# Kernel optimization log

Hardware: AMD Instinct MI355X
Metric: run time of the kernel (lower is better)

The kernel has to match this reference:

```python
import jax, jax.numpy as jnp
import numpy as np

N = 50000
E = 800000
IN_DIM = 256
OUT_DIM = 64
ALPHA = 0.2  # LeakyReLU negative slope
EPS = 9e-15


def setup_inputs() -> dict:
    key = jax.random.key(0)
    k1, k2, k3, k4 = jax.random.split(key, 4)
    x = jax.random.normal(k1, (N, IN_DIM), dtype=jnp.float32)
    edge = jax.random.randint(k2, (2, E), 0, N, dtype=jnp.int32)
    # xavier_normal with gain=1.414
    gain = 1.414
    W = jax.random.normal(k3, (IN_DIM, OUT_DIM), dtype=jnp.float32) * (gain * np.sqrt(2.0 / (IN_DIM + OUT_DIM)))
    attn = jax.random.normal(k4, (1, 2 * OUT_DIM), dtype=jnp.float32) * (gain * np.sqrt(2.0 / (1 + 2 * OUT_DIM)))
    return {"x": x, "edge": edge, "W": W, "attn": attn}


def reference(x, edge, W, attn):
    n = x.shape[0]
    h = x @ W                                   # [N, D]
    src, dst = edge[0], edge[1]
    d = h.shape[1]
    a_src = attn[0, :d]                         # attn . concat(h_src, h_dst) split
    a_dst = attn[0, d:]
    s = h @ a_src                               # [N]
    t = h @ a_dst                               # [N]
    values = s[src] + t[dst]                    # [E] per-edge attention logits
    edge_e_a = jnp.where(values >= 0, values, ALPHA * values)  # LeakyReLU
    edge_e = jnp.exp(edge_e_a - jnp.max(edge_e_a))              # [E]
    # scatter-sum over destination rows (edge[0] is the output row in spmm)
    e_rowsum = jax.ops.segment_sum(edge_e, src, num_segments=n)[:, None]  # [N,1]
    msgs = edge_e[:, None] * h[dst]             # [E, D] gathered messages
    h_prime = jax.ops.segment_sum(msgs, src, num_segments=n)              # [N, D]
    h_prime = h_prime / (e_rowsum + EPS)
    return h_prime
```

## Files before the change

kernel.cpp:

```cpp
#include <hip/hip_runtime.h>
#include <stdint.h>

#define NN 50000
#define NE 800000
#define KDIM 256
#define DDIM 64
#define ALPHA 0.2f
#define EPSV 9e-15f

#define NBIN 512
#define BSPAN 98
#define SPAN2 49
#define BCAP 2048
#define HCAP 1024
#define PBLK 256
#define EPB 3125
#define GEMM_BLOCKS 512
#define FGRID (PBLK + GEMM_BLOCKS)

#define O_S    0
#define O_T    50000
#define O_HB   100000
#define O_WB   1700000
#define O_BIN  1708192
#define O_EBUF 1708704

typedef __bf16 bf16x8 __attribute__((ext_vector_type(8)));
typedef float f32x4 __attribute__((ext_vector_type(4)));

__device__ __forceinline__ ushort f2bf(float f) {
    uint32_t u = __float_as_uint(f);
    return (ushort)((u + 0x7fffu + ((u >> 16) & 1u)) >> 16);
}
__device__ __forceinline__ float bf2f(ushort u) {
    return __uint_as_float(((uint32_t)u) << 16);
}
__device__ __forceinline__ uint binof(uint src) {
    return (src * 85599u) >> 23;
}

__global__ __launch_bounds__(256) void k_prep(const float* __restrict__ W,
                                              uint* __restrict__ BINCNT,
                                              uint4* __restrict__ WB) {
    const int g = blockIdx.x * 256 + threadIdx.x;
    if (g < NBIN) BINCNT[g] = 0u;
    if (g < 2048) {
        int ts = g >> 6;
        int ln = g & 63;
        int s = ts >> 2, t = ts & 3;
        int q = ln >> 4, c = ln & 15;
        union { ushort us[8]; uint4 v; } pk;
#pragma unroll
        for (int j = 0; j < 8; ++j) {
            int k = s * 32 + q * 8 + j;
            pk.us[j] = f2bf(W[k * DDIM + t * 16 + c]);
        }
        WB[g] = pk.v;
    }
}

__global__ __launch_bounds__(512) void k_fused(const float* __restrict__ X,
                                               const uint4* __restrict__ WB,
                                               const float* __restrict__ attn,
                                               const int* __restrict__ edge,
                                               ushort* __restrict__ HB,
                                               float* __restrict__ S,
                                               float* __restrict__ T,
                                               uint* __restrict__ BINCNT,
                                               uint* __restrict__ EBUF) {
    __shared__ uint4 bsm[2048];

    if (blockIdx.x < PBLK) {
        uint* sm = (uint*)bsm;
        const int CNT0 = 0, BST = 512, GBS = 1024, STG = 1536, SRT = 4672;
        const int tid = threadIdx.x;
        const int p0 = blockIdx.x * EPB;
        for (int b = tid; b < NBIN; b += 512) sm[CNT0 + b] = 0u;
        __syncthreads();
        for (int k = tid; k < EPB; k += 512) {
            uint s = (uint)edge[p0 + k];
            uint d = (uint)edge[NE + p0 + k];
            sm[STG + k] = s | (d << 16);
            atomicAdd(&sm[CNT0 + binof(s)], 1u);
        }
        __syncthreads();
        if (tid < 64) {
            uint carry = 0;
            for (int c = 0; c < 8; ++c) {
                uint v = sm[CNT0 + c * 64 + tid];
                uint incl = v;
#pragma unroll
                for (int m = 1; m < 64; m <<= 1) {
                    uint t = __shfl_up(incl, m, 64);
                    if (tid >= m) incl += t;
                }
                sm[BST + c * 64 + tid] = incl - v + carry;
                carry += __shfl(incl, 63, 64);
            }
        }
        __syncthreads();
        for (int b = tid; b < NBIN; b += 512) {
            uint c = sm[CNT0 + b];
            sm[GBS + b] = c ? atomicAdd(&BINCNT[b], c) : 0u;
            sm[CNT0 + b] = sm[BST + b];
        }
        __syncthreads();
        for (int k = tid; k < EPB; k += 512) {
            uint pk = sm[STG + k];
            uint bin = binof(pk & 0xffffu);
            uint slot = atomicAdd(&sm[CNT0 + bin], 1u);
            sm[SRT + slot] = pk;
        }
        __syncthreads();
        for (int k = tid; k < EPB; k += 512) {
            uint pk = sm[SRT + k];
            uint bin = binof(pk & 0xffffu);
            uint local = (uint)k - sm[BST + bin] + sm[GBS + bin];
            if (local < BCAP) EBUF[bin * BCAP + local] = pk;
        }
        return;
    }

    uint4 wreg[4];
#pragma unroll
    for (int j = 0; j < 4; ++j) wreg[j] = WB[j * 512 + threadIdx.x];
#pragma unroll
    for (int j = 0; j < 4; ++j) bsm[j * 512 + threadIdx.x] = wreg[j];
    __syncthreads();

    const int lane = threadIdx.x & 63;
    const int wave = (blockIdx.x - PBLK) * 8 + (threadIdx.x >> 6);
    const int nwaves = GEMM_BLOCKS * 8;
    const int quad = lane >> 4;
    const int nn = lane & 15;

    float asrc[4], adst[4];
#pragma unroll
    for (int t = 0; t < 4; ++t) {
        asrc[t] = attn[t * 16 + nn];
        adst[t] = attn[DDIM + t * 16 + nn];
    }

    const int MT = NN / 16;
    for (int mt = wave; mt < MT; mt += nwaves) {
        const int row0 = mt * 16;
        const float* xr = X + (size_t)(row0 + nn) * KDIM + quad * 8;
        bf16x8 afrag[8];
#pragma unroll
        for (int s = 0; s < 8; ++s) {
            float4 lo = *reinterpret_cast<const float4*>(xr + s * 32);
            float4 hi = *reinterpret_cast<const float4*>(xr + s * 32 + 4);
            union { uint u[4]; bf16x8 v; } aa;
            asm("v_cvt_pk_bf16_f32 %0, %1, %2"
                : "=v"(aa.u[0]) : "v"(lo.x), "v"(lo.y));
            asm("v_cvt_pk_bf16_f32 %0, %1, %2"
                : "=v"(aa.u[1]) : "v"(lo.z), "v"(lo.w));
            asm("v_cvt_pk_bf16_f32 %0, %1, %2"
                : "=v"(aa.u[2]) : "v"(hi.x), "v"(hi.y));
            asm("v_cvt_pk_bf16_f32 %0, %1, %2"
                : "=v"(aa.u[3]) : "v"(hi.z), "v"(hi.w));
            afrag[s] = aa.v;
        }

        f32x4 acc[4];
#pragma unroll
        for (int t = 0; t < 4; ++t) acc[t] = {0.f, 0.f, 0.f, 0.f};
#pragma unroll
        for (int s = 0; s < 8; ++s)
#pragma unroll
            for (int t = 0; t < 4; ++t) {
                bf16x8 bf = *reinterpret_cast<const bf16x8*>(
                    &bsm[(s * 4 + t) * 64 + lane]);
                acc[t] = __builtin_amdgcn_mfma_f32_16x16x32_bf16(
                    afrag[s], bf, acc[t], 0, 0, 0);
            }

#pragma unroll
        for (int t = 0; t < 4; ++t)
#pragma unroll
            for (int r = 0; r < 4; ++r)
                HB[(size_t)(row0 + quad * 4 + r) * DDIM + t * 16 + nn] =
                    f2bf(acc[t][r]);

        float sp[4], tp[4];
#pragma unroll
        for (int r = 0; r < 4; ++r) { sp[r] = 0.f; tp[r] = 0.f; }
#pragma unroll
        for (int t = 0; t < 4; ++t)
#pragma unroll
            for (int r = 0; r < 4; ++r) {
                sp[r] = fmaf(acc[t][r], asrc[t], sp[r]);
                tp[r] = fmaf(acc[t][r], adst[t], tp[r]);
            }
#pragma unroll
        for (int m = 1; m < 16; m <<= 1)
#pragma unroll
            for (int r = 0; r < 4; ++r) {
                sp[r] += __shfl_xor(sp[r], m, 64);
                tp[r] += __shfl_xor(tp[r], m, 64);
            }
        if (nn == 0) {
#pragma unroll
            for (int r = 0; r < 4; ++r) {
                S[row0 + quad * 4 + r] = sp[r];
                T[row0 + quad * 4 + r] = tp[r];
            }
        }
    }
}

__global__ __launch_bounds__(512) void k_agg(const uint* __restrict__ EBUF,
                                             const uint* __restrict__ BINCNT,
                                             const float* __restrict__ S,
                                             const float* __restrict__ T,
                                             const ushort* __restrict__ HB,
                                             float* __restrict__ out) {
    __shared__ uint2 sDE[HCAP];
    __shared__ uint  cntL[SPAN2];
    __shared__ uint  off[SPAN2 + 1];
    __shared__ uint  cur[SPAN2];
    __shared__ float Sseg[SPAN2];

    const int b = blockIdx.x >> 1;
    const int half = blockIdx.x & 1;
    const int nb0 = b * BSPAN + half * SPAN2;
    const int tid = threadIdx.x;

    if (tid < SPAN2) {
        cntL[tid] = 0u;
        int node = nb0 + tid;
        Sseg[tid] = (node < NN) ? S[node] : 0.f;
    }
    __syncthreads();

    int cnt = (int)BINCNT[b];
    cnt = cnt < BCAP ? cnt : BCAP;
    const uint* eb = EBUF + b * BCAP;

    for (int k = tid; k < cnt; k += 512) {
        int row = (int)(eb[k] & 0xffffu) - nb0;
        if ((unsigned)row < SPAN2) atomicAdd(&cntL[row], 1u);
    }
    __syncthreads();

    if (tid < 64) {
        uint v = (tid < SPAN2) ? cntL[tid] : 0u;
        uint incl = v;
#pragma unroll
        for (int m = 1; m < 64; m <<= 1) {
            uint t = __shfl_up(incl, m, 64);
            if (tid >= m) incl += t;
        }
        if (tid < SPAN2) { off[tid] = incl - v; cur[tid] = incl - v; }
        if (tid == SPAN2 - 1) off[SPAN2] = incl;
    }
    __syncthreads();

    for (int k = tid; k < cnt; k += 512) {
        uint pk = eb[k];
        int row = (int)(pk & 0xffffu) - nb0;
        if ((unsigned)row < SPAN2) {
            float v = Sseg[row] + T[pk >> 16];
            float a = v >= 0.f ? v : ALPHA * v;
            float e = __expf(a);
            uint pos = atomicAdd(&cur[row], 1u);
            sDE[pos] = make_uint2(pk >> 16, __float_as_uint(e));
        }
    }
    __syncthreads();

    const int wv = tid >> 6;
    const int lane = tid & 63;
    const int sub4 = lane >> 4;
    const int c4 = lane & 15;
    const ushort* hb4 = HB + 4 * c4;

    for (int r = wv; r < SPAN2; r += 8) {
        const int start = (int)off[r];
        const int deg = (int)(off[r + 1] - off[r]);
        float a0 = 0.f, a1 = 0.f, a2 = 0.f, a3 = 0.f, rs = 0.f;
        for (int j = 0; j < deg; j += 16) {
            uint dd[4]; float ee[4];
#pragma unroll
            for (int u = 0; u < 4; ++u) {
                int idx = j + 4 * u + sub4;
                int ic = start + (idx < deg ? idx : 0);
                uint2 q = sDE[ic];
                dd[u] = q.x;
                ee[u] = (idx < deg) ? __uint_as_float(q.y) : 0.f;
            }
            __builtin_amdgcn_sched_barrier(0);
            uint2 g[4];
#pragma unroll
            for (int u = 0; u < 4; ++u)
                g[u] = *reinterpret_cast<const uint2*>(
                    hb4 + (size_t)dd[u] * DDIM);
            __builtin_amdgcn_sched_barrier(0);
#pragma unroll
            for (int u = 0; u < 4; ++u) {
                a0 = fmaf(ee[u], bf2f((ushort)(g[u].x & 0xffffu)), a0);
                a1 = fmaf(ee[u], bf2f((ushort)(g[u].x >> 16)), a1);
                a2 = fmaf(ee[u], bf2f((ushort)(g[u].y & 0xffffu)), a2);
                a3 = fmaf(ee[u], bf2f((ushort)(g[u].y >> 16)), a3);
                rs += ee[u];
            }
        }
#pragma unroll
        for (int m = 16; m < 64; m <<= 1) {
            a0 += __shfl_xor(a0, m, 64);
            a1 += __shfl_xor(a1, m, 64);
            a2 += __shfl_xor(a2, m, 64);
            a3 += __shfl_xor(a3, m, 64);
            rs += __shfl_xor(rs, m, 64);
        }
        const int node = nb0 + r;
        if (sub4 == 0 && node < NN) {
            float inv = 1.f / (rs + EPSV);
            float4 o = make_float4(a0 * inv, a1 * inv, a2 * inv, a3 * inv);
            *reinterpret_cast<float4*>(out + (size_t)node * DDIM + 4 * c4) = o;
        }
    }
}

extern "C" void kernel_launch(void* const* d_in, const int* in_sizes, int n_in,
                              void* d_out, int out_size, void* d_ws, size_t ws_size,
                              hipStream_t stream) {
    const float* X    = (const float*)d_in[0];
    const int*   edge = (const int*)d_in[1];
    const float* W    = (const float*)d_in[2];
    const float* attn = (const float*)d_in[3];

    uint*   wu = (uint*)d_ws;
    float*  wf = (float*)d_ws;
    float*  S      = wf + O_S;
    float*  T      = wf + O_T;
    ushort* HB     = (ushort*)(wu + O_HB);
    uint4*  WB     = (uint4*)(wu + O_WB);
    uint*   BINCNT = wu + O_BIN;
    uint*   EBUF   = wu + O_EBUF;

    k_prep<<<8, 256, 0, stream>>>(W, BINCNT, WB);
    k_fused<<<FGRID, 512, 0, stream>>>(X, WB, attn, edge, HB, S, T, BINCNT, EBUF);
    k_agg<<<NBIN * 2, 512, 0, stream>>>(EBUF, BINCNT, S, T, HB, (float*)d_out);
}
```

Baseline: 122.8 us.

## Drop local sort in edge binning and double gather unroll in aggregation

The partition blocks no longer compute a prefix scan and local counting sort before writing edges to global bins. Each edge now takes its global slot directly from a shared atomic cursor seeded with the global bin offset, which removes one scan, two barriers and a shared-memory pass. Writes to EBUF become less contiguous and in-bin order becomes nondeterministic. Separately, the aggregation loop issues eight gathers per iteration instead of four, raising memory-level parallelism at the cost of more registers.

Result: slower. 126.4 us (+2.9%).

```diff
diff --git a/kernel.cpp b/kernel.cpp
--- a/kernel.cpp
+++ b/kernel.cpp
@@ -72,7 +72,7 @@
 
     if (blockIdx.x < PBLK) {
         uint* sm = (uint*)bsm;
-        const int CNT0 = 0, BST = 512, GBS = 1024, STG = 1536, SRT = 4672;
+        const int CNT0 = 0, CUR = 512, STG = 1024;
         const int tid = threadIdx.x;
         const int p0 = blockIdx.x * EPB;
         for (int b = tid; b < NBIN; b += 512) sm[CNT0 + b] = 0u;
@@ -84,39 +84,16 @@
             atomicAdd(&sm[CNT0 + binof(s)], 1u);
         }
         __syncthreads();
-        if (tid < 64) {
-            uint carry = 0;
-            for (int c = 0; c < 8; ++c) {
-                uint v = sm[CNT0 + c * 64 + tid];
-                uint incl = v;
-#pragma unroll
-                for (int m = 1; m < 64; m <<= 1) {
-                    uint t = __shfl_up(incl, m, 64);
-                    if (tid >= m) incl += t;
-                }
-                sm[BST + c * 64 + tid] = incl - v + carry;
-                carry += __shfl(incl, 63, 64);
-            }
-        }
-        __syncthreads();
         for (int b = tid; b < NBIN; b += 512) {
             uint c = sm[CNT0 + b];
-            sm[GBS + b] = c ? atomicAdd(&BINCNT[b], c) : 0u;
-            sm[CNT0 + b] = sm[BST + b];
+            sm[CUR + b] = c ? atomicAdd(&BINCNT[b], c) : 0u;
         }
         __syncthreads();
         for (int k = tid; k < EPB; k += 512) {
             uint pk = sm[STG + k];
             uint bin = binof(pk & 0xffffu);
-            uint slot = atomicAdd(&sm[CNT0 + bin], 1u);
-            sm[SRT + slot] = pk;
-        }
-        __syncthreads();
-        for (int k = tid; k < EPB; k += 512) {
-            uint pk = sm[SRT + k];
-            uint bin = binof(pk & 0xffffu);
-            uint local = (uint)k - sm[BST + bin] + sm[GBS + bin];
-            if (local < BCAP) EBUF[bin * BCAP + local] = pk;
+            uint slot = atomicAdd(&sm[CUR + bin], 1u);
+            if (slot < BCAP) EBUF[bin * BCAP + slot] = pk;
         }
         return;
     }
@@ -279,10 +256,10 @@
         const int start = (int)off[r];
         const int deg = (int)(off[r + 1] - off[r]);
         float a0 = 0.f, a1 = 0.f, a2 = 0.f, a3 = 0.f, rs = 0.f;
-        for (int j = 0; j < deg; j += 16) {
-            uint dd[4]; float ee[4];
-#pragma unroll
-            for (int u = 0; u < 4; ++u) {
+        for (int j = 0; j < deg; j += 32) {
+            uint dd[8]; float ee[8];
+#pragma unroll
+            for (int u = 0; u < 8; ++u) {
                 int idx = j + 4 * u + sub4;
                 int ic = start + (idx < deg ? idx : 0);
                 uint2 q = sDE[ic];
@@ -290,14 +267,14 @@
                 ee[u] = (idx < deg) ? __uint_as_float(q.y) : 0.f;
             }
             __builtin_amdgcn_sched_barrier(0);
-            uint2 g[4];
-#pragma unroll
-            for (int u = 0; u < 4; ++u)
+            uint2 g[8];
+#pragma unroll
+            for (int u = 0; u < 8; ++u)
                 g[u] = *reinterpret_cast<const uint2*>(
                     hb4 + (size_t)dd[u] * DDIM);
             __builtin_amdgcn_sched_barrier(0);
 #pragma unroll
-            for (int u = 0; u < 4; ++u) {
+            for (int u = 0; u < 8; ++u) {
                 a0 = fmaf(ee[u], bf2f((ushort)(g[u].x & 0xffffu)), a0);
                 a1 = fmaf(ee[u], bf2f((ushort)(g[u].x >> 16)), a1);
                 a2 = fmaf(ee[u], bf2f((ushort)(g[u].y & 0xffffu)), a2);
```

## Distribute edge-binning shards dynamically across all fused blocks via atomic counter

Applied to the files above, without the earlier changes.

Replaces the fixed split, where 256 blocks bin edges and 512 blocks run the GEMM, with a work queue. Every block, including GEMM blocks once their GEMM work is done, grabs 3072-edge shards through a global atomic counter and bins them. This balances the binning work against the GEMM so neither group of blocks sits idle. In exchange it adds an atomic and extra barriers per shard, and GEMM blocks then run binning with the same shared memory.

Result: slower. 125.8 us (+2.5%).

```diff
diff --git a/kernel.cpp b/kernel.cpp
--- a/kernel.cpp
+++ b/kernel.cpp
@@ -14,9 +14,10 @@
 #define BCAP 2048
 #define HCAP 1024
 #define PBLK 256
-#define EPB 3125
 #define GEMM_BLOCKS 512
 #define FGRID (PBLK + GEMM_BLOCKS)
+#define SHSZ 3072
+#define NSH 261
 
 #define O_S    0
 #define O_T    50000
@@ -24,6 +25,7 @@
 #define O_WB   1700000
 #define O_BIN  1708192
 #define O_EBUF 1708704
+#define O_CTR  2757280
 
 typedef __bf16 bf16x8 __attribute__((ext_vector_type(8)));
 typedef float f32x4 __attribute__((ext_vector_type(4)));
@@ -41,9 +43,11 @@
 
 __global__ __launch_bounds__(256) void k_prep(const float* __restrict__ W,
                                               uint* __restrict__ BINCNT,
+                                              uint* __restrict__ CTR,
                                               uint4* __restrict__ WB) {
     const int g = blockIdx.x * 256 + threadIdx.x;
     if (g < NBIN) BINCNT[g] = 0u;
+    if (g == NBIN) CTR[0] = 0u;
     if (g < 2048) {
         int ts = g >> 6;
         int ln = g & 63;
@@ -67,17 +71,116 @@
                                                float* __restrict__ S,
                                                float* __restrict__ T,
                                                uint* __restrict__ BINCNT,
+                                               uint* __restrict__ CTR,
                                                uint* __restrict__ EBUF) {
     __shared__ uint4 bsm[2048];
-
-    if (blockIdx.x < PBLK) {
-        uint* sm = (uint*)bsm;
-        const int CNT0 = 0, BST = 512, GBS = 1024, STG = 1536, SRT = 4672;
-        const int tid = threadIdx.x;
-        const int p0 = blockIdx.x * EPB;
+    const int tid = threadIdx.x;
+
+    if (blockIdx.x >= PBLK) {
+        uint4 wreg[4];
+#pragma unroll
+        for (int j = 0; j < 4; ++j) wreg[j] = WB[j * 512 + tid];
+#pragma unroll
+        for (int j = 0; j < 4; ++j) bsm[j * 512 + tid] = wreg[j];
+        __syncthreads();
+
+        const int lane = tid & 63;
+        const int wave = (blockIdx.x - PBLK) * 8 + (tid >> 6);
+        const int nwaves = GEMM_BLOCKS * 8;
+        const int quad = lane >> 4;
+        const int nn = lane & 15;
+
+        float asrc[4], adst[4];
+#pragma unroll
+        for (int t = 0; t < 4; ++t) {
+            asrc[t] = attn[t * 16 + nn];
+            adst[t] = attn[DDIM + t * 16 + nn];
+        }
+
+        const int MT = NN / 16;
+        for (int mt = wave; mt < MT; mt += nwaves) {
+            const int row0 = mt * 16;
+            const float* xr = X + (size_t)(row0 + nn) * KDIM + quad * 8;
+            bf16x8 afrag[8];
+#pragma unroll
+            for (int s = 0; s < 8; ++s) {
+                float4 lo = *reinterpret_cast<const float4*>(xr + s * 32);
+                float4 hi = *reinterpret_cast<const float4*>(xr + s * 32 + 4);
+                union { uint u[4]; bf16x8 v; } aa;
+                asm("v_cvt_pk_bf16_f32 %0, %1, %2"
+                    : "=v"(aa.u[0]) : "v"(lo.x), "v"(lo.y));
+                asm("v_cvt_pk_bf16_f32 %0, %1, %2"
+                    : "=v"(aa.u[1]) : "v"(lo.z), "v"(lo.w));
+                asm("v_cvt_pk_bf16_f32 %0, %1, %2"
+                    : "=v"(aa.u[2]) : "v"(hi.x), "v"(hi.y));
+                asm("v_cvt_pk_bf16_f32 %0, %1, %2"
+                    : "=v"(aa.u[3]) : "v"(hi.z), "v"(hi.w));
+                afrag[s] = aa.v;
+            }
+
+            f32x4 acc[4];
+#pragma unroll
+            for (int t = 0; t < 4; ++t) acc[t] = {0.f, 0.f, 0.f, 0.f};
+#pragma unroll
+            for (int s = 0; s < 8; ++s)
+#pragma unroll
+                for (int t = 0; t < 4; ++t) {
+                    bf16x8 bf = *reinterpret_cast<const bf16x8*>(
+                        &bsm[(s * 4 + t) * 64 + lane]);
+                    acc[t] = __builtin_amdgcn_mfma_f32_16x16x32_bf16(
+                        afrag[s], bf, acc[t], 0, 0, 0);
+                }
+
+#pragma unroll
+            for (int t = 0; t < 4; ++t)
+#pragma unroll
+                for (int r = 0; r < 4; ++r)
+                    HB[(size_t)(row0 + quad * 4 + r) * DDIM + t * 16 + nn] =
+                        f2bf(acc[t][r]);
+
+            float sp[4], tp[4];
+#pragma unroll
+            for (int r = 0; r < 4; ++r) { sp[r] = 0.f; tp[r] = 0.f; }
+#pragma unroll
+            for (int t = 0; t < 4; ++t)
+#pragma unroll
+                for (int r = 0; r < 4; ++r) {
+                    sp[r] = fmaf(acc[t][r], asrc[t], sp[r]);
+                    tp[r] = fmaf(acc[t][r], adst[t], tp[r]);
+                }
+#pragma unroll
+            for (int m = 1; m < 16; m <<= 1)
+#pragma unroll
+                for (int r = 0; r < 4; ++r) {
+                    sp[r] += __shfl_xor(sp[r], m, 64);
+                    tp[r] += __shfl_xor(tp[r], m, 64);
+                }
+            if (nn == 0) {
+#pragma unroll
+                for (int r = 0; r < 4; ++r) {
+                    S[row0 + quad * 4 + r] = sp[r];
+                    T[row0 + quad * 4 + r] = tp[r];
+                }
+            }
+        }
+        __syncthreads();
+    }
+
+    uint* sm = (uint*)bsm;
+    const int CNT0 = 0, BST = 512, GBS = 1024, STG = 1536, SRT = 4608;
+    const int SHW = 7680;
+
+    for (;;) {
+        if (tid == 0) sm[SHW] = atomicAdd(CTR, 1u);
+        __syncthreads();
+        const uint sh = sm[SHW];
+        if (sh >= NSH) break;
+        const int p0 = (int)sh * SHSZ;
+        const int nv = (NE - p0) < SHSZ ? (NE - p0) : SHSZ;
+
         for (int b = tid; b < NBIN; b += 512) sm[CNT0 + b] = 0u;
         __syncthreads();
-        for (int k = tid; k < EPB; k += 512) {
+        for (int k = tid; k < nv; k += 512) {
             uint s = (uint)edge[p0 + k];
             uint d = (uint)edge[NE + p0 + k];
             sm[STG + k] = s | (d << 16);
@@ -105,107 +208,20 @@
             sm[CNT0 + b] = sm[BST + b];
         }
         __syncthreads();
-        for (int k = tid; k < EPB; k += 512) {
+        for (int k = tid; k < nv; k += 512) {
             uint pk = sm[STG + k];
             uint bin = binof(pk & 0xffffu);
             uint slot = atomicAdd(&sm[CNT0 + bin], 1u);
             sm[SRT + slot] = pk;
         }
         __syncthreads();
-        for (int k = tid; k < EPB; k += 512) {
+        for (int k = tid; k < nv; k += 512) {
             uint pk = sm[SRT + k];
             uint bin = binof(pk & 0xffffu);
             uint local = (uint)k - sm[BST + bin] + sm[GBS + bin];
             if (local < BCAP) EBUF[bin * BCAP + local] = pk;
         }
-        return;
-    }
-
-    uint4 wreg[4];
-#pragma unroll
-    for (int j = 0; j < 4; ++j) wreg[j] = WB[j * 512 + threadIdx.x];
-#pragma unroll
-    for (int j = 0; j < 4; ++j) bsm[j * 512 + threadIdx.x] = wreg[j];
-    __syncthreads();
-
-    const int lane = threadIdx.x & 63;
-    const int wave = (blockIdx.x - PBLK) * 8 + (threadIdx.x >> 6);
-    const int nwaves = GEMM_BLOCKS * 8;
-    const int quad = lane >> 4;
-    const int nn = lane & 15;
-
-    float asrc[4], adst[4];
-#pragma unroll
-    for (int t = 0; t < 4; ++t) {
-        asrc[t] = attn[t * 16 + nn];
-        adst[t] = attn[DDIM + t * 16 + nn];
-    }
-
-    const int MT = NN / 16;
-    for (int mt = wave; mt < MT; mt += nwaves) {
-        const int row0 = mt * 16;
-        const float* xr = X + (size_t)(row0 + nn) * KDIM + quad * 8;
-        bf16x8 afrag[8];
-#pragma unroll
-        for (int s = 0; s < 8; ++s) {
-            float4 lo = *reinterpret_cast<const float4*>(xr + s * 32);
-            float4 hi = *reinterpret_cast<const float4*>(xr + s * 32 + 4);
-            union { uint u[4]; bf16x8 v; } aa;
-            asm("v_cvt_pk_bf16_f32 %0, %1, %2"
-                : "=v"(aa.u[0]) : "v"(lo.x), "v"(lo.y));
-            asm("v_cvt_pk_bf16_f32 %0, %1, %2"
-                : "=v"(aa.u[1]) : "v"(lo.z), "v"(lo.w));
-            asm("v_cvt_pk_bf16_f32 %0, %1, %2"
-                : "=v"(aa.u[2]) : "v"(hi.x), "v"(hi.y));
-            asm("v_cvt_pk_bf16_f32 %0, %1, %2"
-                : "=v"(aa.u[3]) : "v"(hi.z), "v"(hi.w));
-            afrag[s] = aa.v;
-        }
-
-        f32x4 acc[4];
-#pragma unroll
-        for (int t = 0; t < 4; ++t) acc[t] = {0.f, 0.f, 0.f, 0.f};
-#pragma unroll
-        for (int s = 0; s < 8; ++s)
-#pragma unroll
-            for (int t = 0; t < 4; ++t) {
-                bf16x8 bf = *reinterpret_cast<const bf16x8*>(
-                    &bsm[(s * 4 + t) * 64 + lane]);
-                acc[t] = __builtin_amdgcn_mfma_f32_16x16x32_bf16(
-                    afrag[s], bf, acc[t], 0, 0, 0);
-            }
-
-#pragma unroll
-        for (int t = 0; t < 4; ++t)
-#pragma unroll
-            for (int r = 0; r < 4; ++r)
-                HB[(size_t)(row0 + quad * 4 + r) * DDIM + t * 16 + nn] =
-                    f2bf(acc[t][r]);
-
-        float sp[4], tp[4];
-#pragma unroll
-        for (int r = 0; r < 4; ++r) { sp[r] = 0.f; tp[r] = 0.f; }
-#pragma unroll
-        for (int t = 0; t < 4; ++t)
-#pragma unroll
-            for (int r = 0; r < 4; ++r) {
-                sp[r] = fmaf(acc[t][r], asrc[t], sp[r]);
-                tp[r] = fmaf(acc[t][r], adst[t], tp[r]);
-            }
-#pragma unroll
-        for (int m = 1; m < 16; m <<= 1)
-#pragma unroll
-            for (int r = 0; r < 4; ++r) {
-                sp[r] += __shfl_xor(sp[r], m, 64);
-                tp[r] += __shfl_xor(tp[r], m, 64);
-            }
-        if (nn == 0) {
-#pragma unroll
-            for (int r = 0; r < 4; ++r) {
-                S[row0 + quad * 4 + r] = sp[r];
-                T[row0 + quad * 4 + r] = tp[r];
-            }
-        }
+        __syncthreads();
     }
 }
 
@@ -338,8 +354,9 @@
     uint4*  WB     = (uint4*)(wu + O_WB);
     uint*   BINCNT = wu + O_BIN;
     uint*   EBUF   = wu + O_EBUF;
-
-    k_prep<<<8, 256, 0, stream>>>(W, BINCNT, WB);
-    k_fused<<<FGRID, 512, 0, stream>>>(X, WB, attn, edge, HB, S, T, BINCNT, EBUF);
+    uint*   CTR    = wu + O_CTR;
+
+    k_prep<<<8, 256, 0, stream>>>(W, BINCNT, CTR, WB);
+    k_fused<<<FGRID, 512, 0, stream>>>(X, WB, attn, edge, HB, S, T, BINCNT, CTR, EBUF);
     k_agg<<<NBIN * 2, 512, 0, stream>>>(EBUF, BINCNT, S, T, HB, (float*)d_out);
 }
```
